# Kernel optimization log

Hardware: AMD Instinct MI355X
Metric: run time of the kernel (lower is better)

The kernel has to match this reference:

```python
import jax, jax.numpy as jnp
import numpy as np

N = 50000
E = 800000
F_IN = 128
F_OUT = 128


def setup_inputs() -> dict:
    key = jax.random.key(0)
    ks = jax.random.split(key, 7)
    feature = jax.random.normal(ks[0], (N, F_IN), dtype=jnp.float32)
    self_weight = jax.random.uniform(ks[1], (N, 1), dtype=jnp.float32)
    weight = jax.random.uniform(ks[2], (E,), dtype=jnp.float32)
    src = jax.random.randint(ks[3], (E,), 0, N, dtype=jnp.int32)
    dst = jax.random.randint(ks[4], (E,), 0, N, dtype=jnp.int32)
    W = jax.random.normal(ks[5], (F_OUT, F_IN), dtype=jnp.float32) / np.sqrt(F_IN)
    b = jax.random.normal(ks[6], (F_OUT,), dtype=jnp.float32) * 0.01
    return {"feature": feature, "self_weight": self_weight, "weight": weight,
            "src": src, "dst": dst, "W": W, "b": b}


def reference(feature, self_weight, weight, src, dst, W, b):
    # messages: (w + 1) * h_src  -> [E, F_IN]
    msgs = (weight + 1.0)[:, None] * feature[src]
    # segment-sum into destination nodes -> [N, F_IN]
    agg = jax.ops.segment_sum(msgs, dst, num_segments=N)
    # self-loop affine: h * (self_weight + 1) + aggregated messages
    h = feature * (self_weight + 1.0) + agg
    # final linear: h @ W^T + b
    return h @ W.T + b
```

## Files before the change

### kernel.cpp

```cpp
#include <hip/hip_runtime.h>


#define F 128
#define NPB 32
#define CAPB 1024
#define CHUNK 4096
#define MAXNB 1600

typedef __attribute__((ext_vector_type(8))) short short8;
typedef __attribute__((ext_vector_type(4))) float f32x4;

__device__ inline unsigned short f2b(float f) {
    union { float f; unsigned u; } v; v.f = f;
    unsigned r = (v.u + 0x7fffu + ((v.u >> 16) & 1u)) >> 16;
    return (unsigned short)r;
}
__device__ inline float blo(unsigned u) { union { unsigned u; float f; } x; x.u = u << 16; return x.f; }
__device__ inline float bhi(unsigned u) { union { unsigned u; float f; } x; x.u = u & 0xffff0000u; return x.f; }

struct __align__(8) Edge { unsigned pk; float w; };

__global__ __launch_bounds__(256) void init_kernel(
    const float* __restrict__ feat, const float* __restrict__ W,
    unsigned short* __restrict__ featbf, unsigned short* __restrict__ wbf,
    int* __restrict__ gcur, int n4f, int n4w, int nb)
{
    int i = blockIdx.x * 256 + threadIdx.x;
    if (i < n4f) {
        float4 v = ((const float4*)feat)[i];
        ushort4 h; h.x = f2b(v.x); h.y = f2b(v.y); h.z = f2b(v.z); h.w = f2b(v.w);
        ((ushort4*)featbf)[i] = h;
    } else if (i < n4f + n4w) {
        int j = i - n4f;
        float4 v = ((const float4*)W)[j];
        ushort4 h; h.x = f2b(v.x); h.y = f2b(v.y); h.z = f2b(v.z); h.w = f2b(v.w);
        ((ushort4*)wbf)[j] = h;
    } else if (i - n4f - n4w < nb) {
        gcur[i - n4f - n4w] = 0;
    }
}

__global__ __launch_bounds__(256) void gemm_scatter(
    const unsigned short* __restrict__ featbf, const unsigned short* __restrict__ wbf,
    const int* __restrict__ dst, const int* __restrict__ src,
    const float* __restrict__ weight,
    unsigned short* __restrict__ g, int* __restrict__ gcur,
    Edge* __restrict__ sorted, int M, int E, int SB, int NB)
{
    __shared__ __align__(16) char smem[128 * 136 * 2];
    const int tid = threadIdx.x;

    if ((int)blockIdx.x >= SB) {
        unsigned short* Wl = (unsigned short*)smem;
        const int row0 = ((int)blockIdx.x - SB) * 64;

        for (int i = tid; i < 2048; i += 256) {
            int r = i >> 4, c8 = i & 15;
            *(uint4*)&Wl[r * 136 + c8 * 8] = *(const uint4*)&wbf[r * 128 + c8 * 8];
        }
        __syncthreads();

        const int lane = tid & 63, wid = tid >> 6;
        const int m = lane & 15, quad = lane >> 4;
        const int rbase = wid * 16;
        int rr = row0 + rbase + m; if (rr >= M) rr = M - 1;
        const unsigned short* frow = featbf + (size_t)rr * F;

        short8 afrag[4];
#pragma unroll
        for (int kk = 0; kk < 4; ++kk)
            afrag[kk] = *(const short8*)&frow[kk * 32 + quad * 8];

        f32x4 acc[8];
#pragma unroll
        for (int t = 0; t < 8; ++t) acc[t] = (f32x4){0.f, 0.f, 0.f, 0.f};

#pragma unroll
        for (int kk = 0; kk < 4; ++kk) {
            const int k0 = kk * 32 + quad * 8;
#pragma unroll
            for (int t = 0; t < 8; ++t) {
                short8 bfrag = *(const short8*)&Wl[(t * 16 + m) * 136 + k0];
                acc[t] = __builtin_amdgcn_mfma_f32_16x16x32_bf16(afrag[kk], bfrag, acc[t], 0, 0, 0);
            }
        }

#pragma unroll
        for (int reg = 0; reg < 4; ++reg) {
            int r = row0 + rbase + quad * 4 + reg;
            if (r < M) {
#pragma unroll
                for (int t = 0; t < 8; ++t)
                    g[(size_t)r * F + t * 16 + m] = f2b(acc[t][reg]);
            }
        }
    } else {
        int* hist  = (int*)smem;
        int* lbase = hist + MAXNB;
        const int e0 = (int)blockIdx.x * CHUNK;

        for (int i = tid; i < NB; i += 256) hist[i] = 0;
        __syncthreads();
#pragma unroll
        for (int j = 0; j < CHUNK / 256; ++j) {
            int e = e0 + j * 256 + tid;
            if (e < E) atomicAdd(&hist[dst[e] >> 5], 1);
        }
        __syncthreads();
        for (int i = tid; i < NB; i += 256) {
            int c = hist[i];
            lbase[i] = c ? atomicAdd(&gcur[i], c) : 0;
            hist[i] = 0;
        }
        __syncthreads();
#pragma unroll
        for (int j = 0; j < CHUNK / 256; ++j) {
            int e = e0 + j * 256 + tid;
            if (e < E) {
                int d = dst[e];
                int bkt = d >> 5;
                int pos = lbase[bkt] + atomicAdd(&hist[bkt], 1);
                if (pos < CAPB) {
                    Edge ed;
                    ed.pk = (unsigned)src[e] | ((unsigned)(d & 31) << 16);
                    ed.w = weight[e] + 1.0f;
                    sorted[(size_t)bkt * CAPB + pos] = ed;
                }
            }
        }
    }
}

__global__ __launch_bounds__(256) void bucket_gather(
    const unsigned short* __restrict__ g, const Edge* __restrict__ sorted,
    const int* __restrict__ gcur, const float* __restrict__ sw,
    const float* __restrict__ bvec, float* __restrict__ out, int M)
{
    __shared__ Edge ebuf[CAPB];
    __shared__ int hcnt[NPB];
    __shared__ int off[NPB + 1];
    __shared__ int cur[NPB];

    const int b = blockIdx.x, tid = threadIdx.x;
    int cnt = gcur[b]; if (cnt > CAPB) cnt = CAPB;
    const Edge* sb = sorted + (size_t)b * CAPB;

    if (tid < NPB) hcnt[tid] = 0;
    __syncthreads();
    for (int i = tid; i < cnt; i += 256)
        atomicAdd(&hcnt[sb[i].pk >> 16], 1);
    __syncthreads();
    if (tid < NPB) {
        int v = hcnt[tid];
        int x = v;
#pragma unroll
        for (int s = 1; s < NPB; s <<= 1) {
            int t = __shfl_up(x, s, 64);
            if (tid >= s) x += t;
        }
        off[tid + 1] = x;
        if (tid == 0) off[0] = 0;
        cur[tid] = x - v;
    }
    __syncthreads();
    for (int i = tid; i < cnt; i += 256) {
        Edge e = sb[i];
        int p = atomicAdd(&cur[e.pk >> 16], 1);
        if (p < CAPB) ebuf[p] = e;
    }
    __syncthreads();

    const int grp = tid >> 4, c = tid & 15;
    const float4 b0 = ((const float4*)bvec)[c * 2];
    const float4 b1 = ((const float4*)bvec)[c * 2 + 1];

    for (int nn = grp; nn < NPB; nn += 16) {
        const int node = b * NPB + nn;
        if (node >= M) continue;
        int p = off[nn];
        int pe = off[nn + 1]; if (pe > CAPB) pe = CAPB;

        float acc[8] = {0.f, 0.f, 0.f, 0.f, 0.f, 0.f, 0.f, 0.f};
        for (; p + 1 < pe; p += 2) {
            Edge e0 = ebuf[p], e1 = ebuf[p + 1];
            const uint4 r0 = *(const uint4*)(g + (size_t)(e0.pk & 0xffffu) * F + c * 8);
            const uint4 r1 = *(const uint4*)(g + (size_t)(e1.pk & 0xffffu) * F + c * 8);
            float w0 = e0.w, w1 = e1.w;
            acc[0] = fmaf(w0, blo(r0.x), acc[0]); acc[1] = fmaf(w0, bhi(r0.x), acc[1]);
            acc[2] = fmaf(w0, blo(r0.y), acc[2]); acc[3] = fmaf(w0, bhi(r0.y), acc[3]);
            acc[4] = fmaf(w0, blo(r0.z), acc[4]); acc[5] = fmaf(w0, bhi(r0.z), acc[5]);
            acc[6] = fmaf(w0, blo(r0.w), acc[6]); acc[7] = fmaf(w0, bhi(r0.w), acc[7]);
            acc[0] = fmaf(w1, blo(r1.x), acc[0]); acc[1] = fmaf(w1, bhi(r1.x), acc[1]);
            acc[2] = fmaf(w1, blo(r1.y), acc[2]); acc[3] = fmaf(w1, bhi(r1.y), acc[3]);
            acc[4] = fmaf(w1, blo(r1.z), acc[4]); acc[5] = fmaf(w1, bhi(r1.z), acc[5]);
            acc[6] = fmaf(w1, blo(r1.w), acc[6]); acc[7] = fmaf(w1, bhi(r1.w), acc[7]);
        }
        if (p < pe) {
            Edge e0 = ebuf[p];
            const uint4 r0 = *(const uint4*)(g + (size_t)(e0.pk & 0xffffu) * F + c * 8);
            float w0 = e0.w;
            acc[0] = fmaf(w0, blo(r0.x), acc[0]); acc[1] = fmaf(w0, bhi(r0.x), acc[1]);
            acc[2] = fmaf(w0, blo(r0.y), acc[2]); acc[3] = fmaf(w0, bhi(r0.y), acc[3]);
            acc[4] = fmaf(w0, blo(r0.z), acc[4]); acc[5] = fmaf(w0, bhi(r0.z), acc[5]);
            acc[6] = fmaf(w0, blo(r0.w), acc[6]); acc[7] = fmaf(w0, bhi(r0.w), acc[7]);
        }

        const uint4 sr = *(const uint4*)(g + (size_t)node * F + c * 8);
        const float s = sw[node] + 1.0f;
        float4 o0, o1;
        o0.x = fmaf(s, blo(sr.x), b0.x) + acc[0];
        o0.y = fmaf(s, bhi(sr.x), b0.y) + acc[1];
        o0.z = fmaf(s, blo(sr.y), b0.z) + acc[2];
        o0.w = fmaf(s, bhi(sr.y), b0.w) + acc[3];
        o1.x = fmaf(s, blo(sr.z), b1.x) + acc[4];
        o1.y = fmaf(s, bhi(sr.z), b1.y) + acc[5];
        o1.z = fmaf(s, blo(sr.w), b1.z) + acc[6];
        o1.w = fmaf(s, bhi(sr.w), b1.w) + acc[7];
        float4* o = (float4*)(out + (size_t)node * F + c * 8);
        o[0] = o0; o[1] = o1;
    }
}

extern "C" void kernel_launch(void* const* d_in, const int* in_sizes, int n_in,
                              void* d_out, int out_size, void* d_ws, size_t ws_size,
                              hipStream_t stream) {
    const float* feat   = (const float*)d_in[0];
    const float* sw     = (const float*)d_in[1];
    const float* weight = (const float*)d_in[2];
    const int*   src    = (const int*)  d_in[3];
    const int*   dst    = (const int*)  d_in[4];
    const float* W      = (const float*)d_in[5];
    const float* b      = (const float*)d_in[6];
    float* out = (float*)d_out;

    const int M = in_sizes[1];
    const int E = in_sizes[2];
    const int NB = (M + NPB - 1) / NPB;
    const int GB = (M + 63) / 64;
    const int SB = (E + CHUNK - 1) / CHUNK;

    char* ws = (char*)d_ws;
    size_t og    = 0;
    size_t ofbf  = ((og   + (size_t)M * F * 2) + 255) & ~(size_t)255;
    size_t owbf  = ((ofbf + (size_t)M * F * 2) + 255) & ~(size_t)255;
    size_t ocur  = ((owbf + (size_t)F * F * 2) + 255) & ~(size_t)255;
    size_t osort = ((ocur + (size_t)NB * 4) + 255) & ~(size_t)255;

    unsigned short* g      = (unsigned short*)(ws + og);
    unsigned short* featbf = (unsigned short*)(ws + ofbf);
    unsigned short* wbf    = (unsigned short*)(ws + owbf);
    int*  gcur   = (int*)(ws + ocur);
    Edge* sorted = (Edge*)(ws + osort);

    const int n4f = M * F / 4, n4w = F * F / 4;
    const int initN = n4f + n4w + NB;
    init_kernel<<<(initN + 255) / 256, 256, 0, stream>>>(
        feat, W, featbf, wbf, gcur, n4f, n4w, NB);
    gemm_scatter<<<SB + GB, 256, 0, stream>>>(
        featbf, wbf, dst, src, weight, g, gcur, sorted, M, E, SB, NB);
    bucket_gather<<<NB, 256, 0, stream>>>(g, sorted, gcur, sw, b, out, M);
}
```

Measured before the change: 146.8 us.

## Fuse bf16 conversion into GEMM blocks and unroll gather loop by four

Removes the separate init kernel that converted features and W to bf16. The GEMM blocks now load fp32 feature rows and W directly and convert them in registers or when staging into LDS. The cursor reset becomes a memset. The gather loop also processes four edges per iteration instead of two, for more memory-level parallelism. The cost is that each GEMM block re-converts all of W and holds more registers.

```diff
diff --git a/kernel.cpp b/kernel.cpp
--- a/kernel.cpp
+++ b/kernel.cpp
@@ -20,28 +20,8 @@
 
 struct __align__(8) Edge { unsigned pk; float w; };
 
-__global__ __launch_bounds__(256) void init_kernel(
+__global__ __launch_bounds__(256) void gemm_scatter(
     const float* __restrict__ feat, const float* __restrict__ W,
-    unsigned short* __restrict__ featbf, unsigned short* __restrict__ wbf,
-    int* __restrict__ gcur, int n4f, int n4w, int nb)
-{
-    int i = blockIdx.x * 256 + threadIdx.x;
-    if (i < n4f) {
-        float4 v = ((const float4*)feat)[i];
-        ushort4 h; h.x = f2b(v.x); h.y = f2b(v.y); h.z = f2b(v.z); h.w = f2b(v.w);
-        ((ushort4*)featbf)[i] = h;
-    } else if (i < n4f + n4w) {
-        int j = i - n4f;
-        float4 v = ((const float4*)W)[j];
-        ushort4 h; h.x = f2b(v.x); h.y = f2b(v.y); h.z = f2b(v.z); h.w = f2b(v.w);
-        ((ushort4*)wbf)[j] = h;
-    } else if (i - n4f - n4w < nb) {
-        gcur[i - n4f - n4w] = 0;
-    }
-}
-
-__global__ __launch_bounds__(256) void gemm_scatter(
-    const unsigned short* __restrict__ featbf, const unsigned short* __restrict__ wbf,
     const int* __restrict__ dst, const int* __restrict__ src,
     const float* __restrict__ weight,
     unsigned short* __restrict__ g, int* __restrict__ gcur,
@@ -54,22 +34,39 @@
         unsigned short* Wl = (unsigned short*)smem;
         const int row0 = ((int)blockIdx.x - SB) * 64;
 
-        for (int i = tid; i < 2048; i += 256) {
-            int r = i >> 4, c8 = i & 15;
-            *(uint4*)&Wl[r * 136 + c8 * 8] = *(const uint4*)&wbf[r * 128 + c8 * 8];
-        }
-        __syncthreads();
-
         const int lane = tid & 63, wid = tid >> 6;
         const int m = lane & 15, quad = lane >> 4;
         const int rbase = wid * 16;
         int rr = row0 + rbase + m; if (rr >= M) rr = M - 1;
-        const unsigned short* frow = featbf + (size_t)rr * F;
+        const float* frow = feat + (size_t)rr * F;
+
+        float4 a32[4][2];
+#pragma unroll
+        for (int kk = 0; kk < 4; ++kk) {
+            a32[kk][0] = *(const float4*)&frow[kk * 32 + quad * 8];
+            a32[kk][1] = *(const float4*)&frow[kk * 32 + quad * 8 + 4];
+        }
+
+        for (int i = tid; i < 4096; i += 256) {
+            int r = i >> 5, c4 = i & 31;
+            float4 v = ((const float4*)W)[i];
+            ushort4 h; h.x = f2b(v.x); h.y = f2b(v.y); h.z = f2b(v.z); h.w = f2b(v.w);
+            *(ushort4*)&Wl[r * 136 + c4 * 4] = h;
+        }
 
         short8 afrag[4];
 #pragma unroll
-        for (int kk = 0; kk < 4; ++kk)
-            afrag[kk] = *(const short8*)&frow[kk * 32 + quad * 8];
+        for (int kk = 0; kk < 4; ++kk) {
+            afrag[kk][0] = (short)f2b(a32[kk][0].x);
+            afrag[kk][1] = (short)f2b(a32[kk][0].y);
+            afrag[kk][2] = (short)f2b(a32[kk][0].z);
+            afrag[kk][3] = (short)f2b(a32[kk][0].w);
+            afrag[kk][4] = (short)f2b(a32[kk][1].x);
+            afrag[kk][5] = (short)f2b(a32[kk][1].y);
+            afrag[kk][6] = (short)f2b(a32[kk][1].z);
+            afrag[kk][7] = (short)f2b(a32[kk][1].w);
+        }
+        __syncthreads();
 
         f32x4 acc[8];
 #pragma unroll
@@ -181,11 +178,13 @@
         int pe = off[nn + 1]; if (pe > CAPB) pe = CAPB;
 
         float acc[8] = {0.f, 0.f, 0.f, 0.f, 0.f, 0.f, 0.f, 0.f};
-        for (; p + 1 < pe; p += 2) {
-            Edge e0 = ebuf[p], e1 = ebuf[p + 1];
+        for (; p + 3 < pe; p += 4) {
+            Edge e0 = ebuf[p], e1 = ebuf[p + 1], e2 = ebuf[p + 2], e3 = ebuf[p + 3];
             const uint4 r0 = *(const uint4*)(g + (size_t)(e0.pk & 0xffffu) * F + c * 8);
             const uint4 r1 = *(const uint4*)(g + (size_t)(e1.pk & 0xffffu) * F + c * 8);
-            float w0 = e0.w, w1 = e1.w;
+            const uint4 r2 = *(const uint4*)(g + (size_t)(e2.pk & 0xffffu) * F + c * 8);
+            const uint4 r3 = *(const uint4*)(g + (size_t)(e3.pk & 0xffffu) * F + c * 8);
+            float w0 = e0.w, w1 = e1.w, w2 = e2.w, w3 = e3.w;
             acc[0] = fmaf(w0, blo(r0.x), acc[0]); acc[1] = fmaf(w0, bhi(r0.x), acc[1]);
             acc[2] = fmaf(w0, blo(r0.y), acc[2]); acc[3] = fmaf(w0, bhi(r0.y), acc[3]);
             acc[4] = fmaf(w0, blo(r0.z), acc[4]); acc[5] = fmaf(w0, bhi(r0.z), acc[5]);
@@ -194,8 +193,16 @@
             acc[2] = fmaf(w1, blo(r1.y), acc[2]); acc[3] = fmaf(w1, bhi(r1.y), acc[3]);
             acc[4] = fmaf(w1, blo(r1.z), acc[4]); acc[5] = fmaf(w1, bhi(r1.z), acc[5]);
             acc[6] = fmaf(w1, blo(r1.w), acc[6]); acc[7] = fmaf(w1, bhi(r1.w), acc[7]);
-        }
-        if (p < pe) {
+            acc[0] = fmaf(w2, blo(r2.x), acc[0]); acc[1] = fmaf(w2, bhi(r2.x), acc[1]);
+            acc[2] = fmaf(w2, blo(r2.y), acc[2]); acc[3] = fmaf(w2, bhi(r2.y), acc[3]);
+            acc[4] = fmaf(w2, blo(r2.z), acc[4]); acc[5] = fmaf(w2, bhi(r2.z), acc[5]);
+            acc[6] = fmaf(w2, blo(r2.w), acc[6]); acc[7] = fmaf(w2, bhi(r2.w), acc[7]);
+            acc[0] = fmaf(w3, blo(r3.x), acc[0]); acc[1] = fmaf(w3, bhi(r3.x), acc[1]);
+            acc[2] = fmaf(w3, blo(r3.y), acc[2]); acc[3] = fmaf(w3, bhi(r3.y), acc[3]);
+            acc[4] = fmaf(w3, blo(r3.z), acc[4]); acc[5] = fmaf(w3, bhi(r3.z), acc[5]);
+            acc[6] = fmaf(w3, blo(r3.w), acc[6]); acc[7] = fmaf(w3, bhi(r3.w), acc[7]);
+        }
+        for (; p < pe; ++p) {
             Edge e0 = ebuf[p];
             const uint4 r0 = *(const uint4*)(g + (size_t)(e0.pk & 0xffffu) * F + c * 8);
             float w0 = e0.w;
@@ -241,22 +248,15 @@
 
     char* ws = (char*)d_ws;
     size_t og    = 0;
-    size_t ofbf  = ((og   + (size_t)M * F * 2) + 255) & ~(size_t)255;
-    size_t owbf  = ((ofbf + (size_t)M * F * 2) + 255) & ~(size_t)255;
-    size_t ocur  = ((owbf + (size_t)F * F * 2) + 255) & ~(size_t)255;
+    size_t ocur  = ((og   + (size_t)M * F * 2) + 255) & ~(size_t)255;
     size_t osort = ((ocur + (size_t)NB * 4) + 255) & ~(size_t)255;
 
-    unsigned short* g      = (unsigned short*)(ws + og);
-    unsigned short* featbf = (unsigned short*)(ws + ofbf);
-    unsigned short* wbf    = (unsigned short*)(ws + owbf);
+    unsigned short* g = (unsigned short*)(ws + og);
     int*  gcur   = (int*)(ws + ocur);
     Edge* sorted = (Edge*)(ws + osort);
 
-    const int n4f = M * F / 4, n4w = F * F / 4;
-    const int initN = n4f + n4w + NB;
-    init_kernel<<<(initN + 255) / 256, 256, 0, stream>>>(
-        feat, W, featbf, wbf, gcur, n4f, n4w, NB);
+    hipMemsetAsync(gcur, 0, (size_t)NB * 4, stream);
     gemm_scatter<<<SB + GB, 256, 0, stream>>>(
-        featbf, wbf, dst, src, weight, g, gcur, sorted, M, E, SB, NB);
+        feat, W, dst, src, weight, g, gcur, sorted, M, E, SB, NB);
     bucket_gather<<<NB, 256, 0, stream>>>(g, sorted, gcur, sw, b, out, M);
 }
```

New measurement: 144.2 us. Within noise of the previous version (-1.8%).
